# Kernel tuning notes

Hardware: AMD Instinct MI355X
Metric: run time of the kernel (lower is better)

## Reference

```python
import jax, jax.numpy as jnp
import numpy as np

B, H, W, C = 8, 56, 56, 256
HEADS = 8      # block-level heads; each branch uses HEADS//2
SPLIT = 7      # split_size
EPS = 1e-5


def _ln(x, g, b):
    m = x.mean(-1, keepdims=True)
    v = ((x - m) ** 2).mean(-1, keepdims=True)
    return (x - m) * jax.lax.rsqrt(v + EPS) * g + b


def _lepe_attn(q, k, v, H_sp, W_sp, heads, cw, cb):
    # q,k,v: [B,H,W,Ch]; cross-shaped window attention with LePE depthwise conv bias
    Bq, Hq, Wq, Ch = q.shape
    hd = Ch // heads
    scale = hd ** -0.5
    nh, nw = Hq // H_sp, Wq // W_sp

    def win(t):  # -> [Bw, heads, L, hd]  (Bw = B*nh*nw, L = H_sp*W_sp)
        t = t.reshape(Bq, nh, H_sp, nw, W_sp, Ch).transpose(0, 1, 3, 2, 4, 5)
        return t.reshape(-1, H_sp * W_sp, heads, hd).transpose(0, 2, 1, 3)

    qw, kw = win(q), win(k)
    # v windows laid out NCHW for the depthwise LePE conv
    vimg = v.reshape(Bq, nh, H_sp, nw, W_sp, Ch).transpose(0, 1, 3, 5, 2, 4).reshape(-1, Ch, H_sp, W_sp)
    lepe = jax.lax.conv_general_dilated(
        vimg, cw, window_strides=(1, 1), padding=((1, 1), (1, 1)),
        feature_group_count=Ch, dimension_numbers=("NCHW", "OIHW", "NCHW"))
    lepe = lepe + cb[None, :, None, None]
    lepe = lepe.reshape(-1, heads, hd, H_sp * W_sp).transpose(0, 1, 3, 2)
    vw = vimg.reshape(-1, heads, hd, H_sp * W_sp).transpose(0, 1, 3, 2)

    attn = jax.nn.softmax(jnp.einsum("whld,whmd->whlm", qw * scale, kw), axis=-1)
    out = jnp.einsum("whlm,whmd->whld", attn, vw) + lepe  # [Bw,heads,L,hd]
    out = out.transpose(0, 2, 1, 3).reshape(-1, H_sp, W_sp, Ch)
    # windows2img
    out = out.reshape(Bq, nh, nw, H_sp, W_sp, Ch).transpose(0, 1, 3, 2, 4, 5).reshape(Bq, Hq, Wq, Ch)
    return out


def setup_inputs() -> dict:
    key = jax.random.key(0)
    ks = jax.random.split(key, 8)
    ch = C // 2
    s = 0.02
    return {
        "x": jax.random.normal(ks[0], (B, H, W, C), jnp.float32),
        "gamma1": jnp.ones((C,), jnp.float32), "beta1": jnp.zeros((C,), jnp.float32),
        "w_qkv": jax.random.normal(ks[1], (C, 3 * C), jnp.float32) * s,
        "lepe_w0": jax.random.normal(ks[2], (ch, 1, 3, 3), jnp.float32) * s,
        "lepe_b0": jnp.zeros((ch,), jnp.float32),
        "lepe_w1": jax.random.normal(ks[3], (ch, 1, 3, 3), jnp.float32) * s,
        "lepe_b1": jnp.zeros((ch,), jnp.float32),
        "w_proj": jax.random.normal(ks[4], (C, C), jnp.float32) * s,
        "b_proj": jnp.zeros((C,), jnp.float32),
        "gamma2": jnp.ones((C,), jnp.float32), "beta2": jnp.zeros((C,), jnp.float32),
        "w_fc1": jax.random.normal(ks[5], (C, 4 * C), jnp.float32) * s,
        "b_fc1": jnp.zeros((4 * C,), jnp.float32),
        "w_fc2": jax.random.normal(ks[6], (4 * C, C), jnp.float32) * s,
        "b_fc2": jnp.zeros((C,), jnp.float32),
    }


def reference(x, gamma1, beta1, w_qkv, lepe_w0, lepe_b0, lepe_w1, lepe_b1,
              w_proj, b_proj, gamma2, beta2, w_fc1, b_fc1, w_fc2, b_fc2):
    Bx, Hx, Wx, Cx = x.shape
    img = _ln(x, gamma1, beta1)
    qkv = (img @ w_qkv).reshape(Bx, Hx, Wx, 3, Cx).transpose(3, 0, 1, 2, 4)
    q, k, v = qkv[0], qkv[1], qkv[2]
    ch = Cx // 2
    heads = HEADS // 2
    # branch 0 (idx=0): H_sp=H, W_sp=split  -> vertical stripes
    x0 = _lepe_attn(q[..., :ch], k[..., :ch], v[..., :ch], Hx, SPLIT, heads, lepe_w0, lepe_b0)
    # branch 1 (idx=1): H_sp=split, W_sp=W  -> horizontal stripes
    x1 = _lepe_attn(q[..., ch:], k[..., ch:], v[..., ch:], SPLIT, Wx, heads, lepe_w1, lepe_b1)
    att = jnp.concatenate([x0, x1], axis=-1) @ w_proj + b_proj
    x = x + att
    h = _ln(x, gamma2, beta2)
    h = jax.nn.gelu(h @ w_fc1 + b_fc1, approximate=False) @ w_fc2 + b_fc2
    return x + h
```

## Files before the change

### kernel.cpp

```cpp
#include <hip/hip_runtime.h>
#include <stdint.h>

typedef __attribute__((ext_vector_type(4))) float  f32x4;
typedef __attribute__((ext_vector_type(8))) __bf16 bf16x8;

#define DEVI static __device__ __forceinline__

DEVI float bf2f_lo(uint32_t u) { union { uint32_t i; float f; } v; v.i = u << 16;          return v.f; }
DEVI float bf2f_hi(uint32_t u) { union { uint32_t i; float f; } v; v.i = u & 0xffff0000u;  return v.f; }
DEVI uint16_t f2bf(float f) {
    union { float f; uint32_t i; } v; v.f = f;
    uint32_t r = v.i + 0x7fffu + ((v.i >> 16) & 1u);
    return (uint16_t)(r >> 16);
}
DEVI void unpack8(uint4 u, float* f) {
    f[0] = bf2f_lo(u.x); f[1] = bf2f_hi(u.x);
    f[2] = bf2f_lo(u.y); f[3] = bf2f_hi(u.y);
    f[4] = bf2f_lo(u.z); f[5] = bf2f_hi(u.z);
    f[6] = bf2f_lo(u.w); f[7] = bf2f_hi(u.w);
}
DEVI void gload_lds16(const uint16_t* gp, uint16_t* lp) {
    __builtin_amdgcn_global_load_lds(
        (const __attribute__((address_space(1))) uint32_t*)gp,
        (__attribute__((address_space(3))) uint32_t*)lp, 16, 0, 0);
}

__global__ __launch_bounds__(256) void wprep(const float* __restrict__ w,
                                             uint16_t* __restrict__ wt, int K, int N) {
    int idx = blockIdx.x * 256 + threadIdx.x;
    if (idx >= K * N) return;
    int k = idx / N, n = idx - k * N;
    wt[(size_t)n * K + k] = f2bf(w[idx]);
}

__global__ __launch_bounds__(256) void ln_kernel(const float* __restrict__ x,
                                                 const float* __restrict__ g,
                                                 const float* __restrict__ be,
                                                 uint16_t* __restrict__ y) {
    int row  = blockIdx.x * 4 + (threadIdx.x >> 6);
    int lane = threadIdx.x & 63;
    const float* xr = x + (size_t)row * 256 + lane * 4;
    f32x4 v = *(const f32x4*)xr;
    float s  = v[0] + v[1] + v[2] + v[3];
    float s2 = v[0]*v[0] + v[1]*v[1] + v[2]*v[2] + v[3]*v[3];
#pragma unroll
    for (int off = 32; off > 0; off >>= 1) {
        s  += __shfl_xor(s, off);
        s2 += __shfl_xor(s2, off);
    }
    float mean = s * (1.f / 256.f);
    float var  = s2 * (1.f / 256.f) - mean * mean;
    float rs   = rsqrtf(var + 1e-5f);
    f32x4 gv = *(const f32x4*)(g  + lane * 4);
    f32x4 bv = *(const f32x4*)(be + lane * 4);
    uint64_t pk = 0;
#pragma unroll
    for (int j = 0; j < 4; ++j) {
        uint64_t b = f2bf((v[j] - mean) * rs * gv[j] + bv[j]);
        pk |= b << (16 * j);
    }
    *(uint64_t*)(y + (size_t)row * 256 + lane * 4) = pk;
}

template <int EPI>
__global__ __launch_bounds__(256) void gemm_bt(const uint16_t* __restrict__ A,
                                               const uint16_t* __restrict__ Bt,
                                               int M, int N, int K,
                                               const float* __restrict__ bias,
                                               const float* __restrict__ resid,
                                               void* __restrict__ outp) {
    __shared__ __align__(16) uint16_t As[2][128 * 32];
    __shared__ __align__(16) uint16_t Bs[2][128 * 32];
    const int tid  = threadIdx.x;
    const int lane = tid & 63;
    const int w    = tid >> 6;
    const int wr   = w >> 1, wc = w & 1;
    const int bm = blockIdx.x, bn = blockIdx.y;
    f32x4 acc[4][4] = {};
    const int nk = K >> 5;
    const int wb = w * 512;

    const int srow = tid >> 2;
    const int hwr  = (srow ^ (srow >> 2)) & 3;
    const size_t ao0 = (size_t)srow * K + (size_t)(((tid & 3) ^ hwr) * 8);
    const size_t ao1 = ao0 + (size_t)64 * K;

    const uint16_t* Abase = A  + (size_t)bm * 128 * K;
    const uint16_t* Bbase = Bt + (size_t)bn * 128 * K;

    auto stage = [&](int buf, int kk) {
        const uint16_t* Ab = Abase + kk * 32;
        const uint16_t* Bb = Bbase + kk * 32;
        gload_lds16(Ab + ao0, &As[buf][wb]);
        gload_lds16(Ab + ao1, &As[buf][wb + 2048]);
        gload_lds16(Bb + ao0, &Bs[buf][wb]);
        gload_lds16(Bb + ao1, &Bs[buf][wb + 2048]);
    };

    stage(0, 0);
    __syncthreads();
    int cur = 0;

    const int li = lane & 15;
    const int rA = wr * 64 + li;
    const int rB = wc * 64 + li;
    const int kx = ((lane >> 4) ^ ((li ^ (li >> 2)) & 3)) * 8;

    for (int kk = 0; kk < nk; ++kk) {
        if (kk + 1 < nk) stage(cur ^ 1, kk + 1);

        bf16x8 af[4], bfr[4];
#pragma unroll
        for (int m = 0; m < 4; ++m)
            af[m] = __builtin_bit_cast(bf16x8,
                     *(const uint4*)&As[cur][(rA + m * 16) * 32 + kx]);
#pragma unroll
        for (int n = 0; n < 4; ++n)
            bfr[n] = __builtin_bit_cast(bf16x8,
                      *(const uint4*)&Bs[cur][(rB + n * 16) * 32 + kx]);
#pragma unroll
        for (int m = 0; m < 4; ++m)
#pragma unroll
            for (int n = 0; n < 4; ++n)
                acc[m][n] = __builtin_amdgcn_mfma_f32_16x16x32_bf16(af[m], bfr[n], acc[m][n], 0, 0, 0);

        __syncthreads();
        cur ^= 1;
    }

    const int row0 = bm * 128 + wr * 64 + ((lane >> 4) * 4);
    const int col0 = bn * 128 + wc * 64 + li;
#pragma unroll
    for (int m = 0; m < 4; ++m) {
#pragma unroll
        for (int n = 0; n < 4; ++n) {
            const int col = col0 + n * 16;
#pragma unroll
            for (int r = 0; r < 4; ++r) {
                const int row = row0 + m * 16 + r;
                float v = acc[m][n][r];
                size_t idx = (size_t)row * N + col;
                if (EPI == 0) {
                    ((uint16_t*)outp)[idx] = f2bf(v);
                } else if (EPI == 1) {
                    ((float*)outp)[idx] = v + bias[col] + resid[idx];
                } else {
                    v += bias[col];
                    float ge = 0.5f * v * (1.0f + erff(v * 0.70710678118654752f));
                    ((uint16_t*)outp)[idx] = f2bf(ge);
                }
            }
        }
    }
}

__global__ __launch_bounds__(64) void attn_mfma(const uint16_t* __restrict__ qkv,
                                                uint16_t* __restrict__ att) {
    __shared__ __align__(16) uint16_t Pl[64 * 40];
    int bid = ((int)blockIdx.x & 7) * 448 + ((int)blockIdx.x >> 3);
    const int sub   = bid % 28;
    const int winl  = bid / 28;
    const int qtile = sub % 7;
    const int head  = sub / 7;
    const int win   = winl & 63;
    const int branch = winl >> 6;
    const int lane = threadIdx.x;
    const int g  = lane >> 4;
    const int li = lane & 15;
    const int b = win >> 3, wp = win & 7;
    const int ch0 = branch * 128 + head * 32;
    const int base0 = b * 3136;
    const int woff  = wp * 7;
    const int toks1 = base0 + wp * 392;

    auto tokof = [&](int l) -> int {
        if (branch == 0) { int r = l / 7; return base0 + r * 56 + woff + (l - r * 7); }
        return toks1 + l;
    };
    const int tok391 = tokof(391);
    const int q0 = qtile * 64;

    bf16x8 qf[4];
#pragma unroll
    for (int nb = 0; nb < 4; ++nb) {
        int ql = q0 + nb * 16 + li; if (ql > 391) ql = 391;
        qf[nb] = __builtin_bit_cast(bf16x8,
                 *(const uint4*)(qkv + (size_t)tokof(ql) * 768 + ch0 + g * 8));
    }

    float m_run[4], s_run[4];
    f32x4 oacc[2][4];
#pragma unroll
    for (int nb = 0; nb < 4; ++nb) {
        m_run[nb] = -1e30f; s_run[nb] = 0.f;
        oacc[0][nb] = (f32x4)0.f; oacc[1][nb] = (f32x4)0.f;
    }
    const float c = 0.25503486f;
    const float THR = 31.368f;

    for (int kt = 0; kt < 13; ++kt) {
        const int kbase = kt * 32;
        bf16x8 kf[2];
#pragma unroll
        for (int mb = 0; mb < 2; ++mb) {
            int kl = kbase + mb * 16 + li; if (kl > 391) kl = 391;
            kf[mb] = __builtin_bit_cast(bf16x8,
                     *(const uint4*)(qkv + (size_t)tokof(kl) * 768 + 256 + ch0 + g * 8));
        }
        uint16_t vg0[8], vg1[8];
        {
            int kl0 = kbase + g * 8;
            int tk, cc = 0;
            if (branch == 0) { int r = kl0 / 7; cc = kl0 - r * 7; tk = base0 + r * 56 + woff + cc; }
            else tk = toks1 + kl0;
#pragma unroll
            for (int j = 0; j < 8; ++j) {
                int t = (kl0 + j > 391) ? tok391 : tk;
                const uint16_t* vp = qkv + (size_t)t * 768 + 512 + ch0 + li;
                vg0[j] = vp[0];
                vg1[j] = vp[16];
                if (branch == 0) { if (++cc == 7) { cc = 0; tk += 50; } else ++tk; }
                else ++tk;
            }
        }
        f32x4 sa[2][4] = {};
#pragma unroll
        for (int mb = 0; mb < 2; ++mb)
#pragma unroll
            for (int nb = 0; nb < 4; ++nb)
                sa[mb][nb] = __builtin_amdgcn_mfma_f32_16x16x32_bf16(kf[mb], qf[nb], sa[mb][nb], 0, 0, 0);
        if (kt == 12) {
#pragma unroll
            for (int nb = 0; nb < 4; ++nb)
#pragma unroll
                for (int r = 0; r < 4; ++r) {
                    if (g >= 2) sa[0][nb][r] = -1e30f;
                    sa[1][nb][r] = -1e30f;
                }
        }
#pragma unroll
        for (int nb = 0; nb < 4; ++nb) {
            float mt = fmaxf(fmaxf(fmaxf(sa[0][nb][0], sa[0][nb][1]), fmaxf(sa[0][nb][2], sa[0][nb][3])),
                             fmaxf(fmaxf(sa[1][nb][0], sa[1][nb][1]), fmaxf(sa[1][nb][2], sa[1][nb][3])));
            mt = fmaxf(mt, __shfl_xor(mt, 16));
            mt = fmaxf(mt, __shfl_xor(mt, 32));
            if (!__all(mt <= m_run[nb] + THR)) {
                float m_new = fmaxf(m_run[nb], mt);
                float corr = exp2f((m_run[nb] - m_new) * c);
                m_run[nb] = m_new;
                s_run[nb] *= corr;
#pragma unroll
                for (int mb = 0; mb < 2; ++mb)
#pragma unroll
                    for (int r = 0; r < 4; ++r) oacc[mb][nb][r] *= corr;
            }
            const float m2 = m_run[nb] * c;
            float psum = 0.f;
            uint32_t pk[4];
#pragma unroll
            for (int mb = 0; mb < 2; ++mb) {
                float p0 = exp2f(fmaf(sa[mb][nb][0], c, -m2));
                float p1 = exp2f(fmaf(sa[mb][nb][1], c, -m2));
                float p2 = exp2f(fmaf(sa[mb][nb][2], c, -m2));
                float p3 = exp2f(fmaf(sa[mb][nb][3], c, -m2));
                psum += (p0 + p1) + (p2 + p3);
                union { __bf16 h[2]; uint32_t u; } ca, cb;
                ca.h[0] = (__bf16)p0; ca.h[1] = (__bf16)p1;
                cb.h[0] = (__bf16)p2; cb.h[1] = (__bf16)p3;
                pk[mb * 2 + 0] = ca.u;
                pk[mb * 2 + 1] = cb.u;
            }
            psum += __shfl_xor(psum, 16);
            psum += __shfl_xor(psum, 32);
            s_run[nb] += psum;
            uint32_t* dst = (uint32_t*)&Pl[(li + 16 * nb) * 40];
            dst[g * 2 + 0] = pk[0];
            dst[g * 2 + 1] = pk[1];
            dst[g * 2 + 8] = pk[2];
            dst[g * 2 + 9] = pk[3];
        }
        union { uint16_t u[8]; bf16x8 v; } cv0, cv1;
#pragma unroll
        for (int j = 0; j < 8; ++j) { cv0.u[j] = vg0[j]; cv1.u[j] = vg1[j]; }
        bf16x8 vf0 = cv0.v, vf1 = cv1.v;
        bf16x8 pf[4];
#pragma unroll
        for (int nb = 0; nb < 4; ++nb)
            pf[nb] = __builtin_bit_cast(bf16x8,
                     *(const uint4*)&Pl[(li + 16 * nb) * 40 + g * 8]);
#pragma unroll
        for (int nb = 0; nb < 4; ++nb) {
            oacc[0][nb] = __builtin_amdgcn_mfma_f32_16x16x32_bf16(vf0, pf[nb], oacc[0][nb], 0, 0, 0);
            oacc[1][nb] = __builtin_amdgcn_mfma_f32_16x16x32_bf16(vf1, pf[nb], oacc[1][nb], 0, 0, 0);
        }
    }
#pragma unroll
    for (int nb = 0; nb < 4; ++nb) {
        int ql = q0 + nb * 16 + li;
        if (ql <= 391) {
            float rn = 1.f / s_run[nb];
            uint16_t* op = att + (size_t)tokof(ql) * 256 + ch0;
#pragma unroll
            for (int mb = 0; mb < 2; ++mb)
#pragma unroll
                for (int r = 0; r < 4; ++r)
                    op[mb * 16 + g * 4 + r] = f2bf(oacc[mb][nb][r] * rn);
        }
    }
}

__global__ __launch_bounds__(256) void lepe_kernel(const uint16_t* __restrict__ qkv,
                                                   const float* __restrict__ lw0,
                                                   const float* __restrict__ lb0,
                                                   const float* __restrict__ lw1,
                                                   const float* __restrict__ lb1,
                                                   uint16_t* __restrict__ att) {
    __shared__ float wl[9][256];
    __shared__ float bl[256];
    {
        int tid = threadIdx.x;
        for (int i = tid; i < 2304; i += 256) {
            int tap = i >> 8, ch = i & 255;
            wl[tap][ch] = (ch < 128) ? lw0[ch * 9 + tap] : lw1[(ch - 128) * 9 + tap];
        }
        bl[tid] = (tid < 128) ? lb0[tid] : lb1[tid - 128];
    }
    __syncthreads();

    int idx = blockIdx.x * 256 + threadIdx.x;
    int t = idx >> 5, cg = idx & 31;
    int ch = cg * 8;
    int branch = ch >> 7;
    int b = t / 3136, rem = t - b * 3136, h = rem / 56, w = rem - h * 56;
    int r0, r1, c0, c1;
    if (branch == 0) { r0 = 0; r1 = 55; int wp = w / 7; c0 = wp * 7; c1 = c0 + 6; }
    else             { int hp = h / 7; r0 = hp * 7; r1 = r0 + 6; c0 = 0; c1 = 55; }

    const uint16_t* vbase = qkv + (size_t)b * 3136 * 768 + 512 + ch;
    float acc[8];
    {
        f32x4 b0 = *(const f32x4*)&bl[ch];
        f32x4 b1 = *(const f32x4*)&bl[ch + 4];
#pragma unroll
        for (int d = 0; d < 4; ++d) { acc[d] = b0[d]; acc[d + 4] = b1[d]; }
    }
#pragma unroll
    for (int dy = -1; dy <= 1; ++dy) {
#pragma unroll
        for (int dx = -1; dx <= 1; ++dx) {
            int hh = h + dy, ww = w + dx;
            float mask = (hh >= r0 && hh <= r1 && ww >= c0 && ww <= c1) ? 1.f : 0.f;
            int hc = min(max(hh, r0), r1), wc = min(max(ww, c0), c1);
            uint4 u = *(const uint4*)(vbase + (size_t)(hc * 56 + wc) * 768);
            float vv[8]; unpack8(u, vv);
            const int tap = (dy + 1) * 3 + (dx + 1);
            f32x4 w0 = *(const f32x4*)&wl[tap][ch];
            f32x4 w1 = *(const f32x4*)&wl[tap][ch + 4];
#pragma unroll
            for (int d = 0; d < 4; ++d) {
                acc[d]     += (mask * w0[d]) * vv[d];
                acc[d + 4] += (mask * w1[d]) * vv[d + 4];
            }
        }
    }
    uint16_t* ap = att + (size_t)t * 256 + ch;
    uint4 a = *(const uint4*)ap;
    float av[8]; unpack8(a, av);
    uint16_t ob[8];
#pragma unroll
    for (int d = 0; d < 8; ++d) ob[d] = f2bf(av[d] + acc[d]);
    *(uint4*)ap = *(const uint4*)ob;
}

extern "C" void kernel_launch(void* const* d_in, const int* in_sizes, int n_in,
                              void* d_out, int out_size, void* d_ws, size_t ws_size,
                              hipStream_t stream) {
    const float* x      = (const float*)d_in[0];
    const float* g1     = (const float*)d_in[1];
    const float* be1    = (const float*)d_in[2];
    const float* w_qkv  = (const float*)d_in[3];
    const float* lw0    = (const float*)d_in[4];
    const float* lb0    = (const float*)d_in[5];
    const float* lw1    = (const float*)d_in[6];
    const float* lb1    = (const float*)d_in[7];
    const float* w_proj = (const float*)d_in[8];
    const float* b_proj = (const float*)d_in[9];
    const float* g2     = (const float*)d_in[10];
    const float* be2    = (const float*)d_in[11];
    const float* w_fc1  = (const float*)d_in[12];
    const float* b_fc1  = (const float*)d_in[13];
    const float* w_fc2  = (const float*)d_in[14];
    const float* b_fc2  = (const float*)d_in[15];
    float* out = (float*)d_out;

    char* p = (char*)d_ws;
    auto carve = [&](size_t bytes) -> char* {
        char* q = p; p += (bytes + 255) & ~(size_t)255; return q;
    };
    uint16_t* lnb    = (uint16_t*)carve((size_t)25088 * 256 * 2);
    uint16_t* qkvh   = (uint16_t*)carve((size_t)25088 * 1024 * 2);
    uint16_t* attb   = (uint16_t*)carve((size_t)25088 * 256 * 2);
    float*    x1     = (float*)   carve((size_t)25088 * 256 * 4);
    uint16_t* wqkvT  = (uint16_t*)carve((size_t)768 * 256 * 2);
    uint16_t* wprojT = (uint16_t*)carve((size_t)256 * 256 * 2);
    uint16_t* wfc1T  = (uint16_t*)carve((size_t)1024 * 256 * 2);
    uint16_t* wfc2T  = (uint16_t*)carve((size_t)256 * 1024 * 2);

    wprep<<<768,  256, 0, stream>>>(w_qkv,  wqkvT,  256, 768);
    wprep<<<256,  256, 0, stream>>>(w_proj, wprojT, 256, 256);
    wprep<<<1024, 256, 0, stream>>>(w_fc1,  wfc1T,  256, 1024);
    wprep<<<1024, 256, 0, stream>>>(w_fc2,  wfc2T,  1024, 256);

    ln_kernel<<<6272, 256, 0, stream>>>(x, g1, be1, lnb);
    gemm_bt<0><<<dim3(196, 6), 256, 0, stream>>>(lnb, wqkvT, 25088, 768, 256,
                                                 nullptr, nullptr, qkvh);
    attn_mfma<<<3584, 64, 0, stream>>>(qkvh, attb);
    lepe_kernel<<<3136, 256, 0, stream>>>(qkvh, lw0, lb0, lw1, lb1, attb);
    gemm_bt<1><<<dim3(196, 2), 256, 0, stream>>>(attb, wprojT, 25088, 256, 256,
                                                 b_proj, x, x1);
    ln_kernel<<<6272, 256, 0, stream>>>(x1, g2, be2, lnb);
    gemm_bt<2><<<dim3(196, 8), 256, 0, stream>>>(lnb, wfc1T, 25088, 1024, 256,
                                                 b_fc1, nullptr, qkvh);
    gemm_bt<1><<<dim3(196, 2), 256, 0, stream>>>(qkvh, wfc2T, 25088, 256, 1024,
                                                 b_fc2, x1, out);
}
```

Baseline: 310.9 us.

## Split attention key loop across two waves and merge softmax partials in LDS

The attention kernel now launches two wavefronts per block. Each processes alternating 32-key tiles with its own online-softmax state and private P buffer. At the end, wave 1 writes its running max, sum and output accumulators to shared memory, and wave 0 rescales and combines them before writing. This shortens the serial per-block key loop and adds latency hiding, at the cost of an LDS merge, two barriers and extra exp work.

```diff
diff --git a/kernel.cpp b/kernel.cpp
--- a/kernel.cpp
+++ b/kernel.cpp
@@ -154,9 +154,9 @@
     }
 }
 
-__global__ __launch_bounds__(64) void attn_mfma(const uint16_t* __restrict__ qkv,
-                                                uint16_t* __restrict__ att) {
-    __shared__ __align__(16) uint16_t Pl[64 * 40];
+__global__ __launch_bounds__(128) void attn_mfma(const uint16_t* __restrict__ qkv,
+                                                 uint16_t* __restrict__ att) {
+    __shared__ __align__(16) uint16_t Pl[2][64 * 40];
     int bid = ((int)blockIdx.x & 7) * 448 + ((int)blockIdx.x >> 3);
     const int sub   = bid % 28;
     const int winl  = bid / 28;
@@ -164,7 +164,8 @@
     const int head  = sub / 7;
     const int win   = winl & 63;
     const int branch = winl >> 6;
-    const int lane = threadIdx.x;
+    const int wv   = threadIdx.x >> 6;
+    const int lane = threadIdx.x & 63;
     const int g  = lane >> 4;
     const int li = lane & 15;
     const int b = win >> 3, wp = win & 7;
@@ -198,7 +199,7 @@
     const float c = 0.25503486f;
     const float THR = 31.368f;
 
-    for (int kt = 0; kt < 13; ++kt) {
+    for (int kt = wv; kt < 13; kt += 2) {
         const int kbase = kt * 32;
         bf16x8 kf[2];
 #pragma unroll
@@ -273,7 +274,7 @@
             psum += __shfl_xor(psum, 16);
             psum += __shfl_xor(psum, 32);
             s_run[nb] += psum;
-            uint32_t* dst = (uint32_t*)&Pl[(li + 16 * nb) * 40];
+            uint32_t* dst = (uint32_t*)&Pl[wv][(li + 16 * nb) * 40];
             dst[g * 2 + 0] = pk[0];
             dst[g * 2 + 1] = pk[1];
             dst[g * 2 + 8] = pk[2];
@@ -287,24 +288,48 @@
 #pragma unroll
         for (int nb = 0; nb < 4; ++nb)
             pf[nb] = __builtin_bit_cast(bf16x8,
-                     *(const uint4*)&Pl[(li + 16 * nb) * 40 + g * 8]);
+                     *(const uint4*)&Pl[wv][(li + 16 * nb) * 40 + g * 8]);
 #pragma unroll
         for (int nb = 0; nb < 4; ++nb) {
             oacc[0][nb] = __builtin_amdgcn_mfma_f32_16x16x32_bf16(vf0, pf[nb], oacc[0][nb], 0, 0, 0);
             oacc[1][nb] = __builtin_amdgcn_mfma_f32_16x16x32_bf16(vf1, pf[nb], oacc[1][nb], 0, 0, 0);
         }
     }
-#pragma unroll
-    for (int nb = 0; nb < 4; ++nb) {
-        int ql = q0 + nb * 16 + li;
-        if (ql <= 391) {
-            float rn = 1.f / s_run[nb];
+
+    float* mbuf = (float*)&Pl[0][0];
+    __syncthreads();
+    if (wv == 1) {
+        float* dst = mbuf + lane * 40;
+#pragma unroll
+        for (int nb = 0; nb < 4; ++nb) { dst[nb] = m_run[nb]; dst[4 + nb] = s_run[nb]; }
+#pragma unroll
+        for (int mb = 0; mb < 2; ++mb)
+#pragma unroll
+            for (int nb = 0; nb < 4; ++nb)
+#pragma unroll
+                for (int r = 0; r < 4; ++r)
+                    dst[8 + mb * 16 + nb * 4 + r] = oacc[mb][nb][r];
+    }
+    __syncthreads();
+    if (wv == 0) {
+        const float* src = mbuf + lane * 40;
+#pragma unroll
+        for (int nb = 0; nb < 4; ++nb) {
+            int ql = q0 + nb * 16 + li;
+            if (ql > 391) continue;
+            float m1 = src[nb], s1 = src[4 + nb];
+            float M  = fmaxf(m_run[nb], m1);
+            float a0 = exp2f((m_run[nb] - M) * c);
+            float a1 = exp2f((m1 - M) * c);
+            float rn = 1.f / (s_run[nb] * a0 + s1 * a1);
             uint16_t* op = att + (size_t)tokof(ql) * 256 + ch0;
 #pragma unroll
             for (int mb = 0; mb < 2; ++mb)
 #pragma unroll
-                for (int r = 0; r < 4; ++r)
-                    op[mb * 16 + g * 4 + r] = f2bf(oacc[mb][nb][r] * rn);
+                for (int r = 0; r < 4; ++r) {
+                    float o = oacc[mb][nb][r] * a0 + src[8 + mb * 16 + nb * 4 + r] * a1;
+                    op[mb * 16 + g * 4 + r] = f2bf(o * rn);
+                }
         }
     }
 }
@@ -414,7 +439,7 @@
     ln_kernel<<<6272, 256, 0, stream>>>(x, g1, be1, lnb);
     gemm_bt<0><<<dim3(196, 6), 256, 0, stream>>>(lnb, wqkvT, 25088, 768, 256,
                                                  nullptr, nullptr, qkvh);
-    attn_mfma<<<3584, 64, 0, stream>>>(qkvh, attb);
+    attn_mfma<<<3584, 128, 0, stream>>>(qkvh, attb);
     lepe_kernel<<<3136, 256, 0, stream>>>(qkvh, lw0, lb0, lw1, lb1, attb);
     gemm_bt<1><<<dim3(196, 2), 256, 0, stream>>>(attb, wprojT, 25088, 256, 256,
                                                  b_proj, x, x1);
```

Result: no change. 315.9 us (+1.6%).
